# Kernel tuning notes

Hardware: AMD Instinct MI355X
Metric: run time of the kernel (lower is better)

## Reference

```python
import jax, jax.numpy as jnp
import numpy as np
import math

B, N, D, H = 4, 2048, 256, 4
DH = D // H
EPS = 1e-8


def setup_inputs() -> dict:
    key = jax.random.key(0)
    ks = jax.random.split(key, 8)
    x = jax.random.normal(ks[0], (B, N, D), dtype=jnp.float32)
    # RoPE rotation freqs: exp(i * pos * inv_freq), stored as (cos, sin) pairs -> [N, DH//2, 2]
    d2 = DH // 2
    inv_freq = 1.0 / (10000.0 ** (jnp.arange(d2, dtype=jnp.float32) / d2))
    ang = jnp.arange(N, dtype=jnp.float32)[:, None] * inv_freq[None, :]
    freqs = jnp.stack([jnp.cos(ang), jnp.sin(ang)], axis=-1)  # [N, d2, 2]
    s = 0.02
    g = jnp.ones((D,), dtype=jnp.float32)
    w_qkv = jax.random.normal(ks[1], (D, 3 * D), dtype=jnp.float32) * s
    b_qkv = jnp.zeros((3 * D,), dtype=jnp.float32)
    w_out = jax.random.normal(ks[2], (D, D), dtype=jnp.float32) * s
    b_out = jnp.zeros((D,), dtype=jnp.float32)
    w_gate = jax.random.normal(ks[3], (D, D), dtype=jnp.float32) * s
    b_gate = jnp.zeros((D,), dtype=jnp.float32)
    return {"x": x, "freqs": freqs, "g": g, "w_qkv": w_qkv, "b_qkv": b_qkv,
            "w_out": w_out, "b_out": b_out, "w_gate": w_gate, "b_gate": b_gate}


def _zcrmsnorm(x, g):
    x0 = x - jnp.mean(x, axis=-1, keepdims=True)
    rms = jnp.sqrt(jnp.mean(x0 * x0, axis=-1, keepdims=True) + EPS)
    return x0 / rms * g


def _rope(q, freqs):
    # q: [B,H,N,DH]; freqs: [N,DH//2,2] (cos,sin). Complex multiply on adjacent pairs.
    b, h, n, dh = q.shape
    qp = q.reshape(b, h, n, dh // 2, 2)
    cos = freqs[:n, :, 0][None, None]  # [1,1,N,d2]
    sin = freqs[:n, :, 1][None, None]
    q0, q1 = qp[..., 0], qp[..., 1]
    out = jnp.stack([q0 * cos - q1 * sin, q0 * sin + q1 * cos], axis=-1)
    return out.reshape(b, h, n, dh)


def reference(x, freqs, g, w_qkv, b_qkv, w_out, b_out, w_gate, b_gate):
    b, n, d = x.shape
    h = _zcrmsnorm(x, g)
    qkv = (h @ w_qkv + b_qkv).reshape(b, n, 3, H, DH)
    qkv = jnp.transpose(qkv, (2, 0, 3, 1, 4))  # [3,B,H,N,DH]
    q, k, v = qkv[0], qkv[1], qkv[2]
    q = _rope(q, freqs)
    k = _rope(k, freqs)
    scores = jnp.einsum('bhqd,bhkd->bhqk', q, k) / math.sqrt(DH)
    attn = jax.nn.softmax(scores, axis=-1)  # dropout is identity in eval
    y = jnp.einsum('bhqk,bhkd->bhqd', attn, v)
    y = jnp.transpose(y, (0, 2, 1, 3)).reshape(b, n, d)
    y = y @ w_out + b_out
    gate = jax.nn.sigmoid(h @ w_gate + b_gate)
    return x + gate * y
```

## Files before the change

kernel.cpp:

```cpp
#include <hip/hip_runtime.h>

typedef unsigned short u16;
typedef unsigned int u32;
typedef short short8 __attribute__((ext_vector_type(8)));
typedef float f32x4 __attribute__((ext_vector_type(4)));
typedef float f32x16 __attribute__((ext_vector_type(16)));

#define B_ 4
#define N_ 2048
#define D_ 256
#define H_ 4
#define DH_ 64
#define BN_ 8192

__device__ inline float b2f(u16 u) {
    union { u32 i; float f; } v; v.i = ((u32)u) << 16; return v.f;
}
__device__ inline u16 f2b(float f) {
    union { float f; u32 i; } v; v.f = f;
    return (u16)((v.i + 0x8000u) >> 16);
}
__device__ inline u32 pkbf(float a, float b) {
    union { float f; u32 i; } ua, ub; ua.f = a; ub.f = b;
    return __builtin_amdgcn_perm(ub.i + 0x8000u, ua.i + 0x8000u, 0x07060302u);
}
__device__ inline f32x4 mfma16(short8 a, short8 b, f32x4 c) {
    return __builtin_amdgcn_mfma_f32_16x16x32_bf16(a, b, c, 0, 0, 0);
}
__device__ inline f32x16 mfma32(short8 a, short8 b, f32x16 c) {
    return __builtin_amdgcn_mfma_f32_32x32x16_bf16(a, b, c, 0, 0, 0);
}

#define QSCALE 0.18033688f

__global__ __launch_bounds__(256) void gemm_front(
    const u16* __restrict__ A, const u16* __restrict__ BT,
    const float* __restrict__ b_qkv, const float* __restrict__ b_gate,
    const float* __restrict__ freqs,
    u16* __restrict__ Qb, u16* __restrict__ Kb,
    u16* __restrict__ VT, u16* __restrict__ gatb)
{
    const int tid = threadIdx.x;
    const int wave = tid >> 6, lane = tid & 63;
    const int ln15 = lane & 15, quad = lane >> 4;
    const int by = blockIdx.y;
    const int m0 = blockIdx.x * 128 + (wave & 1) * 64;
    const int n0 = by * 128 + (wave >> 1) * 64;

    const f32x4 zero = {0.f, 0.f, 0.f, 0.f};
    f32x4 acc[4][4];
    #pragma unroll
    for (int i = 0; i < 4; ++i)
        #pragma unroll
        for (int j = 0; j < 4; ++j) acc[i][j] = zero;

    #pragma unroll
    for (int k0 = 0; k0 < 256; k0 += 32) {
        const int koff = k0 + quad * 8;
        short8 a[4], b[4];
        #pragma unroll
        for (int i = 0; i < 4; ++i)
            a[i] = *(const short8*)(A + (size_t)(m0 + i * 16 + ln15) * 256 + koff);
        #pragma unroll
        for (int j = 0; j < 4; ++j)
            b[j] = *(const short8*)(BT + (size_t)(n0 + j * 16 + ln15) * 256 + koff);
        #pragma unroll
        for (int i = 0; i < 4; ++i)
            #pragma unroll
            for (int j = 0; j < 4; ++j)
                acc[i][j] = mfma16(a[i], b[j], acc[i][j]);
    }

    if (by < 4) {
        #pragma unroll
        for (int j = 0; j < 4; ++j) {
            const int c  = n0 + j * 16 + ln15;
            const int hh = (c >> 6) & 3;
            const int dh = c & 63;
            const int d2 = dh >> 1;
            const bool isQ = (c < 256);
            const bool ev  = ((dh & 1) == 0);
            const float bv = b_qkv[c];
            u16* dst = isQ ? Qb : Kb;
            #pragma unroll
            for (int i = 0; i < 4; ++i) {
                const int r = m0 + i * 16 + quad * 4;
                #pragma unroll
                for (int rg = 0; rg < 4; ++rg) {
                    const int t = r + rg;
                    const int n = t & 2047, b = t >> 11;
                    float v = acc[i][j][rg] + bv;
                    float pv = __shfl_xor(v, 1);
                    const float2 cs = *(const float2*)(freqs + (size_t)n * 64 + d2 * 2);
                    float o = ev ? (v * cs.x - pv * cs.y)
                                 : (pv * cs.y + v * cs.x);
                    if (isQ) o *= QSCALE;
                    dst[((size_t)(b * H_ + hh) * N_ + n) * DH_ + dh] = f2b(o);
                }
            }
        }
    } else if (by < 6) {
        #pragma unroll
        for (int j = 0; j < 4; ++j) {
            const int c  = n0 + j * 16 + ln15;
            const int hh = (c >> 6) & 3;
            const int dh = c & 63;
            const float bv = b_qkv[c];
            #pragma unroll
            for (int i = 0; i < 4; ++i) {
                const int r = m0 + i * 16 + quad * 4;
                const int n = r & 2047, b = r >> 11;
                uint2 w;
                w.x = pkbf(acc[i][j][0] + bv, acc[i][j][1] + bv);
                w.y = pkbf(acc[i][j][2] + bv, acc[i][j][3] + bv);
                *(uint2*)(VT + ((size_t)(b * H_ + hh) * DH_ + dh) * N_ + n) = w;
            }
        }
    } else {
        #pragma unroll
        for (int j = 0; j < 4; ++j) {
            const int c  = n0 + j * 16 + ln15;
            const int cg = c - 768;
            const float bv = b_gate[cg];
            #pragma unroll
            for (int i = 0; i < 4; ++i) {
                const int r = m0 + i * 16 + quad * 4;
                #pragma unroll
                for (int rg = 0; rg < 4; ++rg) {
                    float v = acc[i][j][rg] + bv;
                    gatb[(size_t)(r + rg) * 256 + cg] = f2b(1.0f / (1.0f + __expf(-v)));
                }
            }
        }
    }
}

__global__ __launch_bounds__(256) void gemm_thin(
    const u16* __restrict__ A, const u16* __restrict__ BT,
    const float* __restrict__ bias, float* __restrict__ out,
    const float* __restrict__ xin, const u16* __restrict__ gate)
{
    const int tid = threadIdx.x;
    const int wave = tid >> 6, lane = tid & 63;
    const int ln15 = lane & 15, quad = lane >> 4;
    const int m0 = blockIdx.x * 64 + (wave & 1) * 32;
    const int n0 = blockIdx.y * 64 + (wave >> 1) * 32;

    const f32x4 zero = {0.f, 0.f, 0.f, 0.f};
    f32x4 acc[2][2];
    #pragma unroll
    for (int i = 0; i < 2; ++i)
        #pragma unroll
        for (int j = 0; j < 2; ++j) acc[i][j] = zero;

    #pragma unroll
    for (int k0 = 0; k0 < 256; k0 += 32) {
        const int koff = k0 + quad * 8;
        short8 a[2], b[2];
        #pragma unroll
        for (int i = 0; i < 2; ++i)
            a[i] = *(const short8*)(A + (size_t)(m0 + i * 16 + ln15) * 256 + koff);
        #pragma unroll
        for (int j = 0; j < 2; ++j)
            b[j] = *(const short8*)(BT + (size_t)(n0 + j * 16 + ln15) * 256 + koff);
        #pragma unroll
        for (int i = 0; i < 2; ++i)
            #pragma unroll
            for (int j = 0; j < 2; ++j)
                acc[i][j] = mfma16(a[i], b[j], acc[i][j]);
    }

    #pragma unroll
    for (int i = 0; i < 2; ++i) {
        const int r = m0 + i * 16 + quad * 4;
        #pragma unroll
        for (int j = 0; j < 2; ++j) {
            const int c = n0 + j * 16 + ln15;
            const float bv = bias[c];
            #pragma unroll
            for (int rg = 0; rg < 4; ++rg) {
                const size_t idx = (size_t)(r + rg) * 256 + c;
                out[idx] = xin[idx] + b2f(gate[idx]) * (acc[i][j][rg] + bv);
            }
        }
    }
}

__global__ __launch_bounds__(256) void norm_transw_k(
    const float* __restrict__ x, const float* __restrict__ g, u16* __restrict__ h,
    const float* __restrict__ wqkv, const float* __restrict__ wout,
    const float* __restrict__ wgate,
    u16* __restrict__ wqkvT, u16* __restrict__ woutT, u16* __restrict__ wgateT)
{
    if (blockIdx.x < 2048) {
        const int wave = threadIdx.x >> 6, lane = threadIdx.x & 63;
        const int t = blockIdx.x * 4 + wave;
        const float4 u = *(const float4*)(x + (size_t)t * D_ + lane * 4);
        float s  = u.x + u.y + u.z + u.w;
        float s2 = u.x * u.x + u.y * u.y + u.z * u.z + u.w * u.w;
        #pragma unroll
        for (int m = 1; m < 64; m <<= 1) {
            s  += __shfl_xor(s, m);
            s2 += __shfl_xor(s2, m);
        }
        float mean = s * (1.0f / D_);
        float var  = s2 * (1.0f / D_) - mean * mean;
        float rinv = rsqrtf(var + 1e-8f);
        const float4 gv = *(const float4*)(g + lane * 4);
        uint2 o;
        o.x = pkbf((u.x - mean) * rinv * gv.x, (u.y - mean) * rinv * gv.y);
        o.y = pkbf((u.z - mean) * rinv * gv.z, (u.w - mean) * rinv * gv.w);
        *(uint2*)(h + (size_t)t * D_ + lane * 4) = o;
    } else {
        int idx = (blockIdx.x - 2048) * 256 + threadIdx.x;
        if (idx < 768 * 256) {
            int nn = idx >> 8, kk = idx & 255;
            wqkvT[idx] = f2b(wqkv[kk * 768 + nn]);
        }
        idx -= 768 * 256;
        if (idx >= 0 && idx < 256 * 256) {
            int nn = idx >> 8, kk = idx & 255;
            woutT[idx]  = f2b(wout[kk * 256 + nn]);
            wgateT[idx] = f2b(wgate[kk * 256 + nn]);
        }
    }
}

__global__ __launch_bounds__(256, 4) void attn_k(
    const u16* __restrict__ Q, const u16* __restrict__ K,
    const u16* __restrict__ VT, float* __restrict__ Op,
    float* __restrict__ lvp)
{
    __shared__ __align__(16) u16 Ks[2][64][64];
    __shared__ __align__(16) u16 Vs[2][64][64];
    const int tid = threadIdx.x;
    const int wave = tid >> 6, lane = tid & 63;
    const int l31 = lane & 31, hi = lane >> 5;
    const int id = blockIdx.x;
    const int bh   = ((id & 7) << 1) | ((id >> 3) & 1);
    const int quar = (id >> 4) & 3;
    const int q0   = (id >> 6) * 128 + wave * 32;
    const int kt0  = quar * 512;

    const u16* Qh = Q + (size_t)bh * N_ * DH_;
    const u16* Kh = K + (size_t)bh * N_ * DH_;
    const u16* Vh = VT + (size_t)bh * DH_ * N_;

    short8 bq[4];
    #pragma unroll
    for (int kc = 0; kc < 4; ++kc)
        bq[kc] = *(const short8*)(Qh + (size_t)(q0 + l31) * DH_ + kc * 16 + hi * 8);

    f32x16 o0, o1;
    #pragma unroll
    for (int i = 0; i < 16; ++i) { o0[i] = 0.f; o1[i] = 0.f; }
    float lv = 0.f;

    const int srow = tid >> 2, sq4 = tid & 3;
    const int sw = srow & 7;
    const int wg0 = ((sq4) ^ sw) * 8;
    const int wg1 = ((sq4 + 4) ^ sw) * 8;
    const int rsw = l31 & 7;

    {
        uint4 k0 = *(const uint4*)(Kh + (size_t)(kt0 + srow) * DH_ + sq4 * 8);
        uint4 k1 = *(const uint4*)(Kh + (size_t)(kt0 + srow) * DH_ + (sq4 + 4) * 8);
        uint4 v0 = *(const uint4*)(Vh + (size_t)srow * N_ + kt0 + sq4 * 8);
        uint4 v1 = *(const uint4*)(Vh + (size_t)srow * N_ + kt0 + (sq4 + 4) * 8);
        *(uint4*)&Ks[0][srow][wg0] = k0;
        *(uint4*)&Ks[0][srow][wg1] = k1;
        *(uint4*)&Vs[0][srow][wg0] = v0;
        *(uint4*)&Vs[0][srow][wg1] = v1;
    }
    __syncthreads();

    int p = 0;
    for (int c = 0; c < 8; ++c) {
        const bool more = (c + 1 < 8);
        uint4 k0, k1, v0, v1;
        if (more) {
            const int ktn = kt0 + (c + 1) * 64;
            k0 = *(const uint4*)(Kh + (size_t)(ktn + srow) * DH_ + sq4 * 8);
            k1 = *(const uint4*)(Kh + (size_t)(ktn + srow) * DH_ + (sq4 + 4) * 8);
            v0 = *(const uint4*)(Vh + (size_t)srow * N_ + ktn + sq4 * 8);
            v1 = *(const uint4*)(Vh + (size_t)srow * N_ + ktn + (sq4 + 4) * 8);
        }

        #pragma unroll
        for (int g = 0; g < 2; ++g) {
            f32x16 st;
            #pragma unroll
            for (int i = 0; i < 16; ++i) st[i] = 0.f;
            #pragma unroll
            for (int kc = 0; kc < 4; ++kc) {
                const int gran = ((2 * kc + hi) ^ rsw) * 8;
                short8 ka = *(const short8*)&Ks[p][g * 32 + l31][gran];
                st = mfma32(ka, bq[kc], st);
            }
            #pragma unroll
            for (int r = 0; r < 16; ++r) {
                st[r] = exp2f(st[r]);
                lv += st[r];
            }
            #pragma unroll
            for (int kc2 = 0; kc2 < 2; ++kc2) {
                u32 X0, X1, Y0, Y1;
                asm("v_cvt_pk_bf16_f32 %0, %1, %2" : "=v"(X0) : "v"(st[8*kc2+0]), "v"(st[8*kc2+1]));
                asm("v_cvt_pk_bf16_f32 %0, %1, %2" : "=v"(X1) : "v"(st[8*kc2+2]), "v"(st[8*kc2+3]));
                asm("v_cvt_pk_bf16_f32 %0, %1, %2" : "=v"(Y0) : "v"(st[8*kc2+4]), "v"(st[8*kc2+5]));
                asm("v_cvt_pk_bf16_f32 %0, %1, %2" : "=v"(Y1) : "v"(st[8*kc2+6]), "v"(st[8*kc2+7]));
                asm("v_permlane32_swap_b32 %0, %1" : "+v"(X0), "+v"(Y0));
                asm("v_permlane32_swap_b32 %0, %1" : "+v"(X1), "+v"(Y1));
                union { u32 u[4]; short8 s; } bf;
                bf.u[0] = X0; bf.u[1] = X1; bf.u[2] = Y0; bf.u[3] = Y1;
                const int gran = ((2 * (2 * g + kc2) + hi) ^ rsw) * 8;
                short8 va0 = *(const short8*)&Vs[p][l31][gran];
                short8 va1 = *(const short8*)&Vs[p][32 + l31][gran];
                o0 = mfma32(va0, bf.s, o0);
                o1 = mfma32(va1, bf.s, o1);
            }
        }

        if (more) {
            *(uint4*)&Ks[p ^ 1][srow][wg0] = k0;
            *(uint4*)&Ks[p ^ 1][srow][wg1] = k1;
            *(uint4*)&Vs[p ^ 1][srow][wg0] = v0;
            *(uint4*)&Vs[p ^ 1][srow][wg1] = v1;
        }
        __syncthreads();
        p ^= 1;
    }

    lv += __shfl_xor(lv, 32);
    const size_t rowo = ((size_t)(quar * 16 + bh) * N_ + q0 + l31) * DH_;
    #pragma unroll
    for (int go = 0; go < 2; ++go) {
        #pragma unroll
        for (int rq = 0; rq < 4; ++rq) {
            float4 w4;
            if (go == 0) {
                w4.x = o0[rq*4+0]; w4.y = o0[rq*4+1]; w4.z = o0[rq*4+2]; w4.w = o0[rq*4+3];
            } else {
                w4.x = o1[rq*4+0]; w4.y = o1[rq*4+1]; w4.z = o1[rq*4+2]; w4.w = o1[rq*4+3];
            }
            *(float4*)(Op + rowo + go * 32 + 8 * rq + 4 * hi) = w4;
        }
    }
    if (hi == 0) lvp[(size_t)(quar * 16 + bh) * N_ + q0 + l31] = lv;
}

__global__ __launch_bounds__(256) void combine_k(
    const float* __restrict__ Op, const float* __restrict__ lvp,
    u16* __restrict__ yt)
{
    const int t = blockIdx.x * 256 + threadIdx.x;
    const int dh0 = (t & 7) * 8;
    const int q   = (t >> 3) & 2047;
    const int bh  = t >> 14;
    float a[8];
    #pragma unroll
    for (int i = 0; i < 8; ++i) a[i] = 0.f;
    float lsum = 0.f;
    #pragma unroll
    for (int pp = 0; pp < 4; ++pp) {
        const size_t o0 = ((size_t)(pp * 16 + bh) * N_ + q) * DH_ + dh0;
        const float4 u0 = *(const float4*)(Op + o0);
        const float4 u1 = *(const float4*)(Op + o0 + 4);
        a[0] += u0.x; a[1] += u0.y; a[2] += u0.z; a[3] += u0.w;
        a[4] += u1.x; a[5] += u1.y; a[6] += u1.z; a[7] += u1.w;
        lsum += lvp[(size_t)(pp * 16 + bh) * N_ + q];
    }
    const float rl = 1.0f / lsum;
    uint4 w;
    w.x = pkbf(a[0] * rl, a[1] * rl);
    w.y = pkbf(a[2] * rl, a[3] * rl);
    w.z = pkbf(a[4] * rl, a[5] * rl);
    w.w = pkbf(a[6] * rl, a[7] * rl);
    const int b = bh >> 2, h = bh & 3;
    *(uint4*)(yt + ((size_t)b * N_ + q) * D_ + h * 64 + dh0) = w;
}

extern "C" void kernel_launch(void* const* d_in, const int* in_sizes, int n_in,
                              void* d_out, int out_size, void* d_ws, size_t ws_size,
                              hipStream_t stream) {
    const float* x      = (const float*)d_in[0];
    const float* freqs  = (const float*)d_in[1];
    const float* g      = (const float*)d_in[2];
    const float* w_qkv  = (const float*)d_in[3];
    const float* b_qkv  = (const float*)d_in[4];
    const float* w_out  = (const float*)d_in[5];
    const float* b_out  = (const float*)d_in[6];
    const float* w_gate = (const float*)d_in[7];
    const float* b_gate = (const float*)d_in[8];
    float* out = (float*)d_out;

    char* ws = (char*)d_ws;
    size_t off = 0;
    auto carve = [&](size_t nelem) -> u16* {
        u16* p = (u16*)(ws + off);
        off += ((nelem * 2 + 255) / 256) * 256;
        return p;
    };
    u16* h      = carve((size_t)BN_ * D_);
    u16* Qb     = carve((size_t)BN_ * D_);
    u16* Kb     = carve((size_t)BN_ * D_);
    u16* VT     = carve((size_t)BN_ * D_);
    u16* gatb   = carve((size_t)BN_ * D_);
    u16* wqkvT  = carve((size_t)768 * 256);
    u16* wgateT = carve((size_t)256 * 256);
    u16* woutT  = carve((size_t)256 * 256);
    float* Op  = (float*)carve((size_t)4 * 16 * N_ * DH_ * 2);
    float* lvp = (float*)carve((size_t)4 * 16 * N_ * 2);
    u16*   yt  = Qb;

    hipLaunchKernelGGL(norm_transw_k, dim3(3072), dim3(256), 0, stream,
                       x, g, h, w_qkv, w_out, w_gate, wqkvT, woutT, wgateT);
    hipLaunchKernelGGL(gemm_front, dim3(64, 8), dim3(256), 0, stream,
                       h, wqkvT, b_qkv, b_gate, freqs, Qb, Kb, VT, gatb);
    hipLaunchKernelGGL(attn_k, dim3(1024), dim3(256), 0, stream,
                       Qb, Kb, VT, Op, lvp);
    hipLaunchKernelGGL(combine_k, dim3(1024), dim3(256), 0, stream,
                       Op, lvp, yt);
    hipLaunchKernelGGL(gemm_thin, dim3(128, 4), dim3(256), 0, stream,
                       yt, woutT, b_out, out, x, gatb);
}
```

Measured before the change: 148.8 us.

## Fuse split-K attention combine into output GEMM and store partials in bf16

The separate combine kernel is removed. Its reduction of the four key-split attention partials now runs in the prologue of a new output-projection GEMM, which normalises by the summed denominators and stages the bf16 result in shared memory before the MFMA loop. The attention partial outputs are also written as bf16 instead of fp32, halving that intermediate traffic. This saves a launch and the round trip of the y tensor, but adds bf16 rounding of unnormalised partials and uses a 16-row tile that reloads the weight matrix from global memory in every block.

```diff
diff --git a/kernel.cpp b/kernel.cpp
--- a/kernel.cpp
+++ b/kernel.cpp
@@ -135,57 +135,6 @@
     }
 }
 
-__global__ __launch_bounds__(256) void gemm_thin(
-    const u16* __restrict__ A, const u16* __restrict__ BT,
-    const float* __restrict__ bias, float* __restrict__ out,
-    const float* __restrict__ xin, const u16* __restrict__ gate)
-{
-    const int tid = threadIdx.x;
-    const int wave = tid >> 6, lane = tid & 63;
-    const int ln15 = lane & 15, quad = lane >> 4;
-    const int m0 = blockIdx.x * 64 + (wave & 1) * 32;
-    const int n0 = blockIdx.y * 64 + (wave >> 1) * 32;
-
-    const f32x4 zero = {0.f, 0.f, 0.f, 0.f};
-    f32x4 acc[2][2];
-    #pragma unroll
-    for (int i = 0; i < 2; ++i)
-        #pragma unroll
-        for (int j = 0; j < 2; ++j) acc[i][j] = zero;
-
-    #pragma unroll
-    for (int k0 = 0; k0 < 256; k0 += 32) {
-        const int koff = k0 + quad * 8;
-        short8 a[2], b[2];
-        #pragma unroll
-        for (int i = 0; i < 2; ++i)
-            a[i] = *(const short8*)(A + (size_t)(m0 + i * 16 + ln15) * 256 + koff);
-        #pragma unroll
-        for (int j = 0; j < 2; ++j)
-            b[j] = *(const short8*)(BT + (size_t)(n0 + j * 16 + ln15) * 256 + koff);
-        #pragma unroll
-        for (int i = 0; i < 2; ++i)
-            #pragma unroll
-            for (int j = 0; j < 2; ++j)
-                acc[i][j] = mfma16(a[i], b[j], acc[i][j]);
-    }
-
-    #pragma unroll
-    for (int i = 0; i < 2; ++i) {
-        const int r = m0 + i * 16 + quad * 4;
-        #pragma unroll
-        for (int j = 0; j < 2; ++j) {
-            const int c = n0 + j * 16 + ln15;
-            const float bv = bias[c];
-            #pragma unroll
-            for (int rg = 0; rg < 4; ++rg) {
-                const size_t idx = (size_t)(r + rg) * 256 + c;
-                out[idx] = xin[idx] + b2f(gate[idx]) * (acc[i][j][rg] + bv);
-            }
-        }
-    }
-}
-
 __global__ __launch_bounds__(256) void norm_transw_k(
     const float* __restrict__ x, const float* __restrict__ g, u16* __restrict__ h,
     const float* __restrict__ wqkv, const float* __restrict__ wout,
@@ -228,7 +177,7 @@
 
 __global__ __launch_bounds__(256, 4) void attn_k(
     const u16* __restrict__ Q, const u16* __restrict__ K,
-    const u16* __restrict__ VT, float* __restrict__ Op,
+    const u16* __restrict__ VT, u16* __restrict__ Opb,
     float* __restrict__ lvp)
 {
     __shared__ __align__(16) u16 Ks[2][64][64];
@@ -337,47 +286,94 @@
     for (int go = 0; go < 2; ++go) {
         #pragma unroll
         for (int rq = 0; rq < 4; ++rq) {
-            float4 w4;
+            uint2 w;
             if (go == 0) {
-                w4.x = o0[rq*4+0]; w4.y = o0[rq*4+1]; w4.z = o0[rq*4+2]; w4.w = o0[rq*4+3];
+                w.x = pkbf(o0[rq*4+0], o0[rq*4+1]);
+                w.y = pkbf(o0[rq*4+2], o0[rq*4+3]);
             } else {
-                w4.x = o1[rq*4+0]; w4.y = o1[rq*4+1]; w4.z = o1[rq*4+2]; w4.w = o1[rq*4+3];
-            }
-            *(float4*)(Op + rowo + go * 32 + 8 * rq + 4 * hi) = w4;
+                w.x = pkbf(o1[rq*4+0], o1[rq*4+1]);
+                w.y = pkbf(o1[rq*4+2], o1[rq*4+3]);
+            }
+            *(uint2*)(Opb + rowo + go * 32 + 8 * rq + 4 * hi) = w;
         }
     }
     if (hi == 0) lvp[(size_t)(quar * 16 + bh) * N_ + q0 + l31] = lv;
 }
 
-__global__ __launch_bounds__(256) void combine_k(
-    const float* __restrict__ Op, const float* __restrict__ lvp,
-    u16* __restrict__ yt)
+__global__ __launch_bounds__(256) void gemm_out(
+    const u16* __restrict__ Opb, const float* __restrict__ lvp,
+    const u16* __restrict__ BT, const float* __restrict__ bias,
+    float* __restrict__ out, const float* __restrict__ xin,
+    const u16* __restrict__ gate)
 {
-    const int t = blockIdx.x * 256 + threadIdx.x;
-    const int dh0 = (t & 7) * 8;
-    const int q   = (t >> 3) & 2047;
-    const int bh  = t >> 14;
-    float a[8];
-    #pragma unroll
-    for (int i = 0; i < 8; ++i) a[i] = 0.f;
-    float lsum = 0.f;
-    #pragma unroll
-    for (int pp = 0; pp < 4; ++pp) {
-        const size_t o0 = ((size_t)(pp * 16 + bh) * N_ + q) * DH_ + dh0;
-        const float4 u0 = *(const float4*)(Op + o0);
-        const float4 u1 = *(const float4*)(Op + o0 + 4);
-        a[0] += u0.x; a[1] += u0.y; a[2] += u0.z; a[3] += u0.w;
-        a[4] += u1.x; a[5] += u1.y; a[6] += u1.z; a[7] += u1.w;
-        lsum += lvp[(size_t)(pp * 16 + bh) * N_ + q];
-    }
-    const float rl = 1.0f / lsum;
-    uint4 w;
-    w.x = pkbf(a[0] * rl, a[1] * rl);
-    w.y = pkbf(a[2] * rl, a[3] * rl);
-    w.z = pkbf(a[4] * rl, a[5] * rl);
-    w.w = pkbf(a[6] * rl, a[7] * rl);
-    const int b = bh >> 2, h = bh & 3;
-    *(uint4*)(yt + ((size_t)b * N_ + q) * D_ + h * 64 + dh0) = w;
+    __shared__ __align__(16) u16 As[16][264];
+    const int tid = threadIdx.x;
+    const int m0 = blockIdx.x * 16;
+
+    {
+        const int r  = tid >> 4;
+        const int kc = (tid & 15) * 16;
+        const int t  = m0 + r;
+        const int n  = t & 2047, b = t >> 11;
+        const int h  = kc >> 6;
+        const int bh = b * 4 + h;
+        const int dh = kc & 63;
+        float a[16];
+        #pragma unroll
+        for (int i = 0; i < 16; ++i) a[i] = 0.f;
+        float lsum = 0.f;
+        #pragma unroll
+        for (int pp = 0; pp < 4; ++pp) {
+            const size_t base = ((size_t)(pp * 16 + bh) * N_ + n) * DH_ + dh;
+            const uint4 u0 = *(const uint4*)(Opb + base);
+            const uint4 u1 = *(const uint4*)(Opb + base + 8);
+            const u32 uu[8] = {u0.x, u0.y, u0.z, u0.w, u1.x, u1.y, u1.z, u1.w};
+            #pragma unroll
+            for (int i2 = 0; i2 < 8; ++i2) {
+                a[i2 * 2]     += b2f((u16)(uu[i2] & 0xffff));
+                a[i2 * 2 + 1] += b2f((u16)(uu[i2] >> 16));
+            }
+            lsum += lvp[(size_t)(pp * 16 + bh) * N_ + n];
+        }
+        const float rl = 1.0f / lsum;
+        uint4 w0, w1;
+        w0.x = pkbf(a[0] * rl,  a[1] * rl);  w0.y = pkbf(a[2] * rl,  a[3] * rl);
+        w0.z = pkbf(a[4] * rl,  a[5] * rl);  w0.w = pkbf(a[6] * rl,  a[7] * rl);
+        w1.x = pkbf(a[8] * rl,  a[9] * rl);  w1.y = pkbf(a[10] * rl, a[11] * rl);
+        w1.z = pkbf(a[12] * rl, a[13] * rl); w1.w = pkbf(a[14] * rl, a[15] * rl);
+        *(uint4*)&As[r][kc]     = w0;
+        *(uint4*)&As[r][kc + 8] = w1;
+    }
+    __syncthreads();
+
+    const int wave = tid >> 6, lane = tid & 63;
+    const int ln15 = lane & 15, quad = lane >> 4;
+    const int n0 = wave * 64;
+    const f32x4 zero = {0.f, 0.f, 0.f, 0.f};
+    f32x4 acc[4] = {zero, zero, zero, zero};
+
+    #pragma unroll
+    for (int k0 = 0; k0 < 256; k0 += 32) {
+        const int koff = k0 + quad * 8;
+        const short8 a = *(const short8*)&As[ln15][koff];
+        #pragma unroll
+        for (int j = 0; j < 4; ++j) {
+            const short8 bfr = *(const short8*)(BT + (size_t)(n0 + j * 16 + ln15) * 256 + koff);
+            acc[j] = mfma16(a, bfr, acc[j]);
+        }
+    }
+
+    #pragma unroll
+    for (int j = 0; j < 4; ++j) {
+        const int c = n0 + j * 16 + ln15;
+        const float bv = bias[c];
+        const int r = quad * 4;
+        #pragma unroll
+        for (int rg = 0; rg < 4; ++rg) {
+            const size_t idx = (size_t)(m0 + r + rg) * 256 + c;
+            out[idx] = xin[idx] + b2f(gate[idx]) * (acc[j][rg] + bv);
+        }
+    }
 }
 
 extern "C" void kernel_launch(void* const* d_in, const int* in_sizes, int n_in,
@@ -409,18 +405,15 @@
     u16* wqkvT  = carve((size_t)768 * 256);
     u16* wgateT = carve((size_t)256 * 256);
     u16* woutT  = carve((size_t)256 * 256);
-    float* Op  = (float*)carve((size_t)4 * 16 * N_ * DH_ * 2);
+    u16*   Opb = carve((size_t)4 * 16 * N_ * DH_);
     float* lvp = (float*)carve((size_t)4 * 16 * N_ * 2);
-    u16*   yt  = Qb;
 
     hipLaunchKernelGGL(norm_transw_k, dim3(3072), dim3(256), 0, stream,
                        x, g, h, w_qkv, w_out, w_gate, wqkvT, woutT, wgateT);
     hipLaunchKernelGGL(gemm_front, dim3(64, 8), dim3(256), 0, stream,
                        h, wqkvT, b_qkv, b_gate, freqs, Qb, Kb, VT, gatb);
     hipLaunchKernelGGL(attn_k, dim3(1024), dim3(256), 0, stream,
-                       Qb, Kb, VT, Op, lvp);
-    hipLaunchKernelGGL(combine_k, dim3(1024), dim3(256), 0, stream,
-                       Op, lvp, yt);
-    hipLaunchKernelGGL(gemm_thin, dim3(128, 4), dim3(256), 0, stream,
-                       yt, woutT, b_out, out, x, gatb);
-}
+                       Qb, Kb, VT, Opb, lvp);
+    hipLaunchKernelGGL(gemm_out, dim3(512), dim3(256), 0, stream,
+                       Opb, lvp, woutT, b_out, out, x, gatb);
+}
```

After: 147.0 us. No clear change (-1.2%).
